# Kernel optimization log

Hardware: AMD Instinct MI355X
Metric: run time of the kernel (lower is better)

Reference implementation:

```python
import jax, jax.numpy as jnp
import numpy as np

EPS = 1e-7          # K.epsilon()
START_TEMP = 10.0
MIN_TEMP = 0.1
ALPHA = 0.99999


def setup_inputs() -> dict:
    key = jax.random.key(0)
    k1, k2, k3, k4 = jax.random.split(key, 4)
    batch, n_feat, bins, out_dim = 4096, 20000, 64, 256
    X = jax.random.normal(k1, (batch, n_feat), dtype=jnp.float32)
    u = jax.random.normal(k2, (n_feat, bins), dtype=jnp.float32)
    # keras 'uniform' initializer ~ U(-0.05, 0.05)
    tinyW = jax.random.uniform(k3, (bins, out_dim), minval=-0.05, maxval=0.05, dtype=jnp.float32)
    uniform = jax.random.uniform(k4, (out_dim, n_feat), minval=EPS, maxval=1.0, dtype=jnp.float32)
    return {"X": X, "u": u, "tinyW": tinyW, "uniform": uniform}


def reference(X, u, tinyW, uniform):
    # al = softmax(u @ tinyW) over output_dim axis, then transpose -> (D, N)
    al = jax.nn.softmax(jnp.dot(u, tinyW), axis=-1).T            # (D, N)
    logits = jnp.log(10.0 * jnp.clip(al, EPS, 0.9999999))        # (D, N)
    gumbel = -jnp.log(-jnp.log(uniform))                          # (D, N)
    temp = jnp.maximum(MIN_TEMP, START_TEMP * ALPHA)              # one K.update step
    samples = jax.nn.softmax((logits + gumbel) / temp, axis=-1)   # (D, N)

    D, N = samples.shape

    # Greedy global-argmax with row/column suppression (inference path).
    # Each of the D iterations picks the global max of p, marks dl[x, y] = 1,
    # then masks row x and column y with -1 (as the numpy loop does).
    def step(carry, _):
        p, dl = carry
        ind = jnp.argmax(p)            # flat argmax over D*N
        x = ind // N
        y = ind % N
        dl = dl.at[x, y].set(1.0)
        p = p.at[x, :].set(-1.0)
        p = p.at[:, y].set(-1.0)
        return (p, dl), None

    (_, dl), _ = jax.lax.scan(step, (samples, jnp.zeros_like(samples)), None, length=D)
    # After D iterations each row of dl has exactly one 1, so
    # one_hot(argmax(dl, axis=-1)) == dl; selections = dl in inference mode.
    Y = jnp.dot(X, dl.T)               # (batch, D)
    return Y
```

## Files before the change

### kernel.cpp

```cpp
#include <hip/hip_runtime.h>
#include <cmath>
#include <cfloat>
#include <climits>

#define NFEAT 20000
#define DDIM 256
#define KDIM 64
#define SEGN 32
#define NSEG 625
#define SEGP 640

#define LOG2E 1.4426950408889634
#define INVT (1.0 / 9.9999)
#define LOG2_10 3.3219280948873623
#define G2C 0.5287663729448976
#define LO2 -23.253496664211536
#define HI2 -1.4426951130237154e-7

__device__ __forceinline__ double frcp(double a) {
  double r;
  asm("v_rcp_f64 %0, %1" : "=v"(r) : "v"(a));
  r = fma(fma(-a, r, 1.0), r, r);
  r = fma(fma(-a, r, 1.0), r, r);
  return r;
}

__device__ __forceinline__ double fexp2(double x) {
  const double nd = rint(x);
  const double y = (x - nd) * 0.6931471805599453;
  double p = 1.0 / 3628800.0;
  p = fma(p, y, 1.0 / 362880.0);
  p = fma(p, y, 1.0 / 40320.0);
  p = fma(p, y, 1.0 / 5040.0);
  p = fma(p, y, 1.0 / 720.0);
  p = fma(p, y, 1.0 / 120.0);
  p = fma(p, y, 1.0 / 24.0);
  p = fma(p, y, 1.0 / 6.0);
  p = fma(p, y, 0.5);
  p = fma(p, y, 1.0);
  p = fma(p, y, 1.0);
  const int n = (int)nd;
  const double sc = __longlong_as_double((long long)(n + 1023) << 52);
  return p * sc;
}

__device__ __forceinline__ double flog2(double x) {
  const long long b = __double_as_longlong(x);
  int e = (int)(b >> 52) - 1023;
  double m = __longlong_as_double((b & 0xfffffffffffffLL) | 0x3ff0000000000000LL);
  if (m > 1.4142135623730951) { m *= 0.5; e += 1; }
  const double t = (m - 1.0) * frcp(m + 1.0);
  const double w = t * t;
  double p = 1.0 / 13.0;
  p = fma(p, w, 1.0 / 11.0);
  p = fma(p, w, 1.0 / 9.0);
  p = fma(p, w, 1.0 / 7.0);
  p = fma(p, w, 1.0 / 5.0);
  p = fma(p, w, 1.0 / 3.0);
  p = fma(p, w, 1.0);
  return fma((2.0 * LOG2E) * t, p, (double)e);
}

__device__ __forceinline__ double z2_post(double L2raw, float uu) {
  const double L2 = fmin(fmax(L2raw, LO2), HI2);
  const double t = -flog2((double)uu);
  const double g2 = G2C - flog2(t);
  return (LOG2_10 + L2 + g2) * INVT;
}

__device__ __forceinline__ double compute_z2(
    const float* __restrict__ u, const float* __restrict__ W,
    const float* __restrict__ unif, const double* __restrict__ lseN,
    int dd, int n) {
  double acc = 0.0;
  const float* ur = u + (size_t)n * KDIM;
#pragma unroll 8
  for (int k = 0; k < KDIM; ++k)
    acc = fma((double)ur[k] * LOG2E, (double)W[k * DDIM + dd], acc);
  return z2_post(acc - lseN[n], unif[(size_t)dd * NFEAT + n]);
}

__device__ __forceinline__ unsigned long long dkey(double v) {
  const long long b = __double_as_longlong(v);
  const unsigned long long ub = (unsigned long long)b;
  return (b < 0) ? ~ub : (ub | 0x8000000000000000ull);
}

__global__ __launch_bounds__(256) void k_init(double* __restrict__ rowSum,
                                              unsigned long long* __restrict__ rowKey) {
  rowSum[threadIdx.x] = 0.0;
  rowKey[threadIdx.x] = 0ull;
}

__global__ __launch_bounds__(256) void k_seg(
    const float* __restrict__ u, const float* __restrict__ W,
    const float* __restrict__ unif, double* __restrict__ lseN,
    double* __restrict__ segVal, int* __restrict__ segCol,
    double* __restrict__ rowSum, unsigned long long* __restrict__ rowKey) {
  const int s = blockIdx.x;
  const int n0 = s * SEGN;
  const int d = threadIdx.x;
  const int lane = d & 63, w = d >> 6;

  __shared__ __align__(16) double ut2[SEGN][KDIM];
  __shared__ float unT[SEGN][DDIM];
  __shared__ double ssum[4][8];
  __shared__ double lse2s[8];

  for (int i = d; i < SEGN * KDIM; i += 256)
    ut2[i >> 6][i & 63] =
        (double)u[(size_t)(n0 + (i >> 6)) * KDIM + (i & 63)] * LOG2E;
  for (int q = 0; q < SEGN; q += 4) {
    const float4 t = *(const float4*)(unif + (size_t)d * NFEAT + n0 + q);
    unT[q + 0][d] = t.x;
    unT[q + 1][d] = t.y;
    unT[q + 2][d] = t.z;
    unT[q + 3][d] = t.w;
  }
  float wcol[KDIM];
#pragma unroll
  for (int k = 0; k < KDIM; ++k) wcol[k] = W[k * DDIM + d];
  __syncthreads();

  double ssl = 0.0;
  double segm = -INFINITY;
  int segc = -1;

  for (int b0 = 0; b0 < SEGN; b0 += 8) {
    double acc[8];
#pragma unroll
    for (int i = 0; i < 8; ++i) acc[i] = 0.0;
#pragma unroll
    for (int k4 = 0; k4 < 16; ++k4) {
      const int kb = k4 * 4;
      const double w0 = (double)wcol[kb + 0], w1 = (double)wcol[kb + 1];
      const double w2 = (double)wcol[kb + 2], w3 = (double)wcol[kb + 3];
#pragma unroll
      for (int i = 0; i < 8; ++i) {
        const double2 ua = *(const double2*)&ut2[b0 + i][kb];
        const double2 ub = *(const double2*)&ut2[b0 + i][kb + 2];
        acc[i] = fma(ua.x, w0, acc[i]);
        acc[i] = fma(ua.y, w1, acc[i]);
        acc[i] = fma(ub.x, w2, acc[i]);
        acc[i] = fma(ub.y, w3, acc[i]);
      }
    }
    double sl[8];
#pragma unroll
    for (int i = 0; i < 8; ++i) sl[i] = fexp2(acc[i]);
#pragma unroll
    for (int off = 1; off < 64; off <<= 1)
#pragma unroll
      for (int i = 0; i < 8; ++i) sl[i] += __shfl_xor(sl[i], off, 64);
    if (lane == 0)
#pragma unroll
      for (int i = 0; i < 8; ++i) ssum[w][i] = sl[i];
    __syncthreads();
    if (d < 8) {
      const double tot = ssum[0][d] + ssum[1][d] + ssum[2][d] + ssum[3][d];
      const double lz = flog2(tot);
      lse2s[d] = lz;
      lseN[n0 + b0 + d] = lz;
    }
    __syncthreads();
#pragma unroll 2
    for (int i = 0; i < 8; ++i) {
      const double z2 = z2_post(acc[i] - lse2s[i], unT[b0 + i][d]);
      ssl += fexp2(z2);
      if (z2 > segm) { segm = z2; segc = n0 + b0 + i; }
    }
    __syncthreads();
  }
  segVal[(size_t)d * SEGP + s] = segm;
  segCol[(size_t)d * SEGP + s] = segc;
  atomicAdd(&rowSum[d], ssl);
  atomicMax(&rowKey[d], (dkey(segm) & 0xFFFFFFFFFFFF0000ull) |
                            (unsigned long long)(0xFFFF - segc));
}

__global__ __launch_bounds__(64) void k_greedy(
    const float* __restrict__ u, const float* __restrict__ W,
    const float* __restrict__ unif, const double* __restrict__ lseN,
    double* __restrict__ segVal, int* __restrict__ segCol,
    const double* __restrict__ rowSum,
    const unsigned long long* __restrict__ rowKey, int* __restrict__ sel,
    int* __restrict__ selWs) {
  const int lane = threadIdx.x;
  __shared__ double kk[DDIM], sk[DDIM], logLs[DDIM];
  __shared__ int sr[DDIM], sc[DDIM], selL[DDIM];
  __shared__ unsigned int supp[NFEAT / 32];
  for (int i = lane; i < NFEAT / 32; i += 64) supp[i] = 0u;

  double myk[4];
  int myc[4];
#pragma unroll
  for (int i = 0; i < 4; ++i) {
    const int dd = lane + 64 * i;
    const double lL = flog2(rowSum[dd]);
    logLs[dd] = lL;
    const unsigned long long key = rowKey[dd];
    const int col = 0xFFFF - (int)(key & 0xFFFFull);
    const double bv = segVal[(size_t)dd * SEGP + (col >> 5)];
    myk[i] = bv - lL;
    myc[i] = col;
    kk[dd] = myk[i];
  }
  __syncthreads();
#pragma unroll
  for (int i = 0; i < 4; ++i) {
    int dd = lane + 64 * i;
    int rk = 0;
#pragma unroll 4
    for (int j = 0; j < DDIM; ++j) {
      double kj = kk[j];
      if (kj > myk[i] || (kj == myk[i] && j < dd)) ++rk;
    }
    sk[rk] = myk[i];
    sr[rk] = dd;
    sc[rk] = myc[i];
  }
  __syncthreads();

  int pos = 0;
  for (int guard = 0; guard < 4 * DDIM && pos < DDIM; ++guard) {
    const int p = pos + lane;
    const bool valid = p < DDIM;
    int r = -1, c = -1000000 - lane;
    if (valid) { r = sr[p]; c = sc[p]; }
    bool conf = !valid;
    if (valid) conf = (supp[c >> 5] >> (c & 31)) & 1u;
    bool dup = false;
#pragma unroll
    for (int j = 0; j < 63; ++j) {
      int cj = __shfl(c, j, 64);
      if (j < lane && cj == c) dup = true;
    }
    if (valid && dup) conf = true;
    unsigned long long bm = __ballot(conf);
    int fc = bm ? (__ffsll(bm) - 1) : 64;
    if (lane < fc) {
      selL[r] = c;
      atomicOr(&supp[c >> 5], 1u << (c & 31));
    }
    __syncthreads();
    pos += fc;
    if (fc < 64 && pos < DDIM) {
      const int rr = sr[pos];
      double pbv = -INFINITY;
      int pbc = INT_MAX;
      int stale[10];
      int scnt = 0;
#pragma unroll
      for (int i2 = 0; i2 < 10; ++i2) {
        int s2 = lane + 64 * i2;
        if (s2 < NSEG) {
          double v = segVal[(size_t)rr * SEGP + s2];
          int cc = segCol[(size_t)rr * SEGP + s2];
          if (cc >= 0) {
            if ((supp[cc >> 5] >> (cc & 31)) & 1u) stale[scnt++] = s2;
            else if (v > pbv || (v == pbv && cc < pbc)) { pbv = v; pbc = cc; }
          }
        }
      }
      unsigned long long sm2 = __ballot(scnt > 0);
      for (int g2 = 0; g2 < NSEG + 4 && sm2; ++g2) {
        int src = __ffsll(sm2) - 1;
        int cand = (scnt > 0) ? stale[scnt - 1] : 0;
        int s2 = __shfl(cand, src, 64);
        if (lane == src) --scnt;
        int ccol = s2 * SEGN + lane;
        double zv = -INFINITY;
        if (lane < SEGN && !((supp[ccol >> 5] >> (ccol & 31)) & 1u))
          zv = compute_z2(u, W, unif, lseN, rr, ccol);
        int zc = (zv == -INFINITY) ? INT_MAX : ccol;
#pragma unroll
        for (int off = 32; off > 0; off >>= 1) {
          double ov = __shfl_xor(zv, off, 64);
          int oc = __shfl_xor(zc, off, 64);
          if (ov > zv || (ov == zv && oc < zc)) { zv = ov; zc = oc; }
        }
        if (lane == 0) {
          segVal[(size_t)rr * SEGP + s2] = (zc == INT_MAX) ? -INFINITY : zv;
          segCol[(size_t)rr * SEGP + s2] = (zc == INT_MAX) ? -1 : zc;
        }
        if (zc != INT_MAX && (zv > pbv || (zv == pbv && zc < pbc))) {
          pbv = zv;
          pbc = zc;
        }
        sm2 = __ballot(scnt > 0);
      }
#pragma unroll
      for (int off = 32; off > 0; off >>= 1) {
        double ov = __shfl_xor(pbv, off, 64);
        int oc = __shfl_xor(pbc, off, 64);
        if (ov > pbv || (ov == pbv && oc < pbc)) { pbv = ov; pbc = oc; }
      }
      const double knew = pbv - logLs[rr];
      const int cn = pbc;
      int cnt = 0;
      for (int q = pos + 1 + lane; q < DDIM; q += 64) {
        double kq = sk[q];
        int rq = sr[q];
        if (kq > knew || (kq == knew && rq < rr)) ++cnt;
      }
#pragma unroll
      for (int off = 32; off > 0; off >>= 1) cnt += __shfl_xor(cnt, off, 64);
      for (int q0 = pos + 1; q0 <= pos + cnt; q0 += 64) {
        int q = q0 + lane;
        double tk = 0.0;
        int tr = 0, tc = 0;
        bool v2 = q <= pos + cnt;
        if (v2) { tk = sk[q]; tr = sr[q]; tc = sc[q]; }
        __syncthreads();
        if (v2) { sk[q - 1] = tk; sr[q - 1] = tr; sc[q - 1] = tc; }
        __syncthreads();
      }
      if (lane == 0) { sk[pos + cnt] = knew; sr[pos + cnt] = rr; sc[pos + cnt] = cn; }
      __syncthreads();
    }
  }
#pragma unroll
  for (int i = 0; i < 4; ++i) {
    const int v = selL[lane + 64 * i];
    sel[lane + 64 * i] = v;
    if (selWs) selWs[lane + 64 * i] = v;
  }
}

__global__ __launch_bounds__(256) void k_gather_all(
    const float* __restrict__ X, const int* __restrict__ selWs, float* out) {
  const int dd = threadIdx.x;
  const size_t b = (size_t)blockIdx.x;
  out[b * DDIM + dd] = X[b * NFEAT + selWs[dd]];
}

__global__ __launch_bounds__(256) void k_gather(const float* __restrict__ X,
                                                float* out) {
  const int dd = threadIdx.x;
  const size_t b = (size_t)blockIdx.x + 1;
  const int y = __float_as_int(out[dd]);
  out[b * DDIM + dd] = X[b * NFEAT + y];
}

__global__ __launch_bounds__(256) void k_row0(const float* __restrict__ X,
                                              float* out) {
  const int dd = threadIdx.x;
  const int y = __float_as_int(out[dd]);
  const float v = X[y];
  out[dd] = v;
}

extern "C" void kernel_launch(void* const* d_in, const int* in_sizes, int n_in,
                              void* d_out, int out_size, void* d_ws,
                              size_t ws_size, hipStream_t stream) {
  (void)in_sizes; (void)n_in; (void)out_size;
  const float* X = (const float*)d_in[0];
  const float* u = (const float*)d_in[1];
  const float* W = (const float*)d_in[2];
  const float* unif = (const float*)d_in[3];

  char* ob = (char*)d_out;
  int* sel = (int*)ob;
  double* lseN = (double*)(ob + 1024);
  double* rowSum = (double*)(ob + 161024);
  unsigned long long* rowKey = (unsigned long long*)(ob + 163072);
  double* segVal = (double*)(ob + 165120);
  int* segCol = (int*)(ob + 1475840);

  const bool use_ws = (d_ws != nullptr) && (ws_size >= 4096);
  int* selWs = use_ws ? (int*)d_ws : nullptr;

  k_init<<<1, 256, 0, stream>>>(rowSum, rowKey);
  k_seg<<<NSEG, 256, 0, stream>>>(u, W, unif, lseN, segVal, segCol, rowSum,
                                  rowKey);
  k_greedy<<<1, 64, 0, stream>>>(u, W, unif, lseN, segVal, segCol, rowSum,
                                 rowKey, sel, selWs);
  if (use_ws) {
    k_gather_all<<<4096, 256, 0, stream>>>(X, selWs, (float*)d_out);
  } else {
    k_gather<<<4095, 256, 0, stream>>>(X, (float*)d_out);
    k_row0<<<1, 256, 0, stream>>>(X, (float*)d_out);
  }
}
```

Baseline: 623.2 us.

## Stripe row atomics, double-buffer reduction smem, and shorten exp/log polynomials

Row sum and row max atomics are spread over 8 stripes to reduce contention across the 625 segment blocks, and the greedy kernel reduces the stripes. The per-chunk reduction shared buffers are double-buffered so the trailing barrier in the segment loop can be removed. The exp2 and log2 polynomial approximations each drop one term to cut FLOPs, at some risk to precision in near-tie argmax decisions. Scratch offsets in the output buffer are shifted to fit the striped arrays.

```diff
diff --git a/kernel.cpp b/kernel.cpp
--- a/kernel.cpp
+++ b/kernel.cpp
@@ -9,6 +9,7 @@
 #define SEGN 32
 #define NSEG 625
 #define SEGP 640
+#define NSTRIPE 8
 
 #define LOG2E 1.4426950408889634
 #define INVT (1.0 / 9.9999)
@@ -28,8 +29,7 @@
 __device__ __forceinline__ double fexp2(double x) {
   const double nd = rint(x);
   const double y = (x - nd) * 0.6931471805599453;
-  double p = 1.0 / 3628800.0;
-  p = fma(p, y, 1.0 / 362880.0);
+  double p = 1.0 / 362880.0;
   p = fma(p, y, 1.0 / 40320.0);
   p = fma(p, y, 1.0 / 5040.0);
   p = fma(p, y, 1.0 / 720.0);
@@ -51,8 +51,7 @@
   if (m > 1.4142135623730951) { m *= 0.5; e += 1; }
   const double t = (m - 1.0) * frcp(m + 1.0);
   const double w = t * t;
-  double p = 1.0 / 13.0;
-  p = fma(p, w, 1.0 / 11.0);
+  double p = 1.0 / 11.0;
   p = fma(p, w, 1.0 / 9.0);
   p = fma(p, w, 1.0 / 7.0);
   p = fma(p, w, 1.0 / 5.0);
@@ -88,8 +87,11 @@
 
 __global__ __launch_bounds__(256) void k_init(double* __restrict__ rowSum,
                                               unsigned long long* __restrict__ rowKey) {
-  rowSum[threadIdx.x] = 0.0;
-  rowKey[threadIdx.x] = 0ull;
+#pragma unroll
+  for (int j = 0; j < NSTRIPE; ++j) {
+    rowSum[j * DDIM + threadIdx.x] = 0.0;
+    rowKey[j * DDIM + threadIdx.x] = 0ull;
+  }
 }
 
 __global__ __launch_bounds__(256) void k_seg(
@@ -104,8 +106,8 @@
 
   __shared__ __align__(16) double ut2[SEGN][KDIM];
   __shared__ float unT[SEGN][DDIM];
-  __shared__ double ssum[4][8];
-  __shared__ double lse2s[8];
+  __shared__ double ssum[2][4][8];
+  __shared__ double lse2s[2][8];
 
   for (int i = d; i < SEGN * KDIM; i += 256)
     ut2[i >> 6][i & 63] =
@@ -127,6 +129,7 @@
   int segc = -1;
 
   for (int b0 = 0; b0 < SEGN; b0 += 8) {
+    const int pb = (b0 >> 3) & 1;
     double acc[8];
 #pragma unroll
     for (int i = 0; i < 8; ++i) acc[i] = 0.0;
@@ -154,28 +157,30 @@
       for (int i = 0; i < 8; ++i) sl[i] += __shfl_xor(sl[i], off, 64);
     if (lane == 0)
 #pragma unroll
-      for (int i = 0; i < 8; ++i) ssum[w][i] = sl[i];
+      for (int i = 0; i < 8; ++i) ssum[pb][w][i] = sl[i];
     __syncthreads();
     if (d < 8) {
-      const double tot = ssum[0][d] + ssum[1][d] + ssum[2][d] + ssum[3][d];
+      const double tot =
+          ssum[pb][0][d] + ssum[pb][1][d] + ssum[pb][2][d] + ssum[pb][3][d];
       const double lz = flog2(tot);
-      lse2s[d] = lz;
+      lse2s[pb][d] = lz;
       lseN[n0 + b0 + d] = lz;
     }
     __syncthreads();
 #pragma unroll 2
     for (int i = 0; i < 8; ++i) {
-      const double z2 = z2_post(acc[i] - lse2s[i], unT[b0 + i][d]);
+      const double z2 = z2_post(acc[i] - lse2s[pb][i], unT[b0 + i][d]);
       ssl += fexp2(z2);
       if (z2 > segm) { segm = z2; segc = n0 + b0 + i; }
     }
-    __syncthreads();
   }
   segVal[(size_t)d * SEGP + s] = segm;
   segCol[(size_t)d * SEGP + s] = segc;
-  atomicAdd(&rowSum[d], ssl);
-  atomicMax(&rowKey[d], (dkey(segm) & 0xFFFFFFFFFFFF0000ull) |
-                            (unsigned long long)(0xFFFF - segc));
+  const int st = s & (NSTRIPE - 1);
+  atomicAdd(&rowSum[st * DDIM + d], ssl);
+  atomicMax(&rowKey[st * DDIM + d],
+            (dkey(segm) & 0xFFFFFFFFFFFF0000ull) |
+                (unsigned long long)(0xFFFF - segc));
 }
 
 __global__ __launch_bounds__(64) void k_greedy(
@@ -196,9 +201,16 @@
 #pragma unroll
   for (int i = 0; i < 4; ++i) {
     const int dd = lane + 64 * i;
-    const double lL = flog2(rowSum[dd]);
+    double sum = 0.0;
+    unsigned long long key = 0ull;
+#pragma unroll
+    for (int j = 0; j < NSTRIPE; ++j) {
+      sum += rowSum[j * DDIM + dd];
+      const unsigned long long kj = rowKey[j * DDIM + dd];
+      if (kj > key) key = kj;
+    }
+    const double lL = flog2(sum);
     logLs[dd] = lL;
-    const unsigned long long key = rowKey[dd];
     const int col = 0xFFFF - (int)(key & 0xFFFFull);
     const double bv = segVal[(size_t)dd * SEGP + (col >> 5)];
     myk[i] = bv - lL;
@@ -363,9 +375,9 @@
   int* sel = (int*)ob;
   double* lseN = (double*)(ob + 1024);
   double* rowSum = (double*)(ob + 161024);
-  unsigned long long* rowKey = (unsigned long long*)(ob + 163072);
-  double* segVal = (double*)(ob + 165120);
-  int* segCol = (int*)(ob + 1475840);
+  unsigned long long* rowKey = (unsigned long long*)(ob + 177408);
+  double* segVal = (double*)(ob + 193792);
+  int* segCol = (int*)(ob + 1504512);
 
   const bool use_ws = (d_ws != nullptr) && (ws_size >= 4096);
   int* selWs = use_ws ? (int*)d_ws : nullptr;
```

Result: no change. 623.9 us (+0.1%).
